# Kernel tuning notes

Measured on AMD Instinct MI355X. Metric: run time of the kernel, lower is better.

Reference implementation:

```python
import jax, jax.numpy as jnp
import numpy as np

TK, HA = 3, 8          # num_blocks, num_heads
AVGF = 32              # num_submatrices
LN_EPS = 1e-5


def _layernorm(x, g, b):
    m = jnp.mean(x, axis=-1, keepdims=True)
    v = jnp.mean((x - m) ** 2, axis=-1, keepdims=True)
    return (x - m) / jnp.sqrt(v + LN_EPS) * g + b


def setup_inputs() -> dict:
    key = jax.random.key(0)
    ks = jax.random.split(key, 12)
    A, B, T = 16, 128, 512
    M = A * B              # 2048
    Dh = M // HA           # 256
    H = 4 * M              # 8192
    s = 0.05               # scale randn params so activations stay finite
    return {
        "x": jax.random.normal(ks[0], (A, B, T), jnp.float32),
        "weight": jax.random.normal(ks[1], (M, M), jnp.float32) * s,
        "Wq": jax.random.normal(ks[2], (TK, HA, Dh, M), jnp.float32) * s,
        "Wk": jax.random.normal(ks[3], (TK, HA, Dh, M), jnp.float32) * s,
        "Wv": jax.random.normal(ks[4], (TK, HA, Dh, M), jnp.float32) * s,
        "Wo": jax.random.normal(ks[5], (TK, M, M), jnp.float32) * s,
        "ln1_g": jnp.ones((M,), jnp.float32),
        "ln1_b": jnp.zeros((M,), jnp.float32),
        "ln2_g": jnp.ones((M,), jnp.float32),
        "ln2_b": jnp.zeros((M,), jnp.float32),
        "fc1_w": jax.random.normal(ks[6], (H, M), jnp.float32) * 0.02,
        "fc1_b": jnp.zeros((H,), jnp.float32),
        "fc2_w": jax.random.normal(ks[7], (M, H), jnp.float32) * 0.02,
        "fc2_b": jnp.zeros((M,), jnp.float32),
    }


def reference(x, weight, Wq, Wk, Wv, Wo, ln1_g, ln1_b, ln2_g, ln2_b,
              fc1_w, fc1_b, fc2_w, fc2_b):
    A, B, T = x.shape
    M = A * B
    Dh = M // HA
    seg = T // AVGF
    # redefine(): transpose(0,2) -> (T,B,A), segment-average along time, flatten
    xt = jnp.transpose(x, (2, 1, 0))                       # (T, B, A)
    xc = xt.reshape(AVGF, seg, B, A).mean(axis=1)          # (AVGF, B, A)
    xcf = xc.reshape(AVGF, M)                              # (AVGF, M)
    # savespace[i] = weight @ x[i]  + sinusoidal positional bias
    pos = jnp.arange(AVGF, dtype=jnp.float32)[:, None]
    je = jnp.arange(0, M, 2, dtype=jnp.float32)
    ang = pos / (10000.0 ** (2.0 * je / M))                # (AVGF, M/2)
    bias = jnp.zeros((AVGF, M), jnp.float32)
    bias = bias.at[:, 0::2].set(jnp.sin(ang)).at[:, 1::2].set(jnp.cos(ang))
    s0 = xcf @ weight.T + bias                             # (AVGF, M)
    scale = 1.0 / jnp.sqrt(jnp.float32(Dh))

    # Sequential recurrence over tokens: vcum[a] carries the cumulative
    # softmax-weighted V sum (softmax over a scalar == 1) per block/head.
    def step(vcum, s):
        for a in range(TK):
            xn = _layernorm(s, ln1_g, ln1_b)
            q = jnp.einsum('hdm,m->hd', Wq[a], xn)         # (HA, Dh)
            k = jnp.einsum('hdm,m->hd', Wk[a], xn)
            v = jnp.einsum('hdm,m->hd', Wv[a], xn)
            scores = jnp.sum(q * k, axis=-1) * scale       # (HA,) scalars
            w = jax.nn.softmax(scores[:, None], axis=-1)[:, 0]  # ones
            vcum = vcum.at[a].add(w[:, None] * v)
            s = Wo[a] @ vcum[a].reshape(-1) + s
            s = _layernorm(s, ln2_g, ln2_b) + s
            h = jax.nn.gelu(fc1_w @ s + fc1_b, approximate=False)
            s = fc2_w @ h + fc2_b
        return vcum, s

    vcum0 = jnp.zeros((TK, HA, Dh), s0.dtype)
    _, out = jax.lax.scan(step, vcum0, s0)                 # (AVGF, M)
    return out.reshape(AVGF, B, A)
```

## Files before the change

kernel.cpp:

```cpp
#include <hip/hip_runtime.h>
#include <math.h>

typedef __attribute__((ext_vector_type(8))) short short8;
typedef __attribute__((ext_vector_type(4))) float floatx4;

__device__ inline unsigned f2bf1(float f) {
    union { float f; unsigned u; } v; v.f = f;
    return (v.u + 0x8000u) >> 16;
}

__device__ inline short8 pack8(float4 a, float4 b) {
    short8 r;
    r[0] = (short)f2bf1(a.x); r[1] = (short)f2bf1(a.y);
    r[2] = (short)f2bf1(a.z); r[3] = (short)f2bf1(a.w);
    r[4] = (short)f2bf1(b.x); r[5] = (short)f2bf1(b.y);
    r[6] = (short)f2bf1(b.z); r[7] = (short)f2bf1(b.w);
    return r;
}

__device__ inline float gelu1(float x) {
    return 0.5f * x * (1.0f + erff(x * 0.70710678118654752f));
}

__global__ __launch_bounds__(128) void avg_k(const float* __restrict__ x,
                                             float* __restrict__ xcf) {
    int blk = blockIdx.x;
    int a = blk >> 7, b = blk & 127;
    int t = threadIdx.x;
    const float4 v = *(const float4*)(x + ((size_t)a * 128 + b) * 512 + t * 4);
    float s = v.x + v.y + v.z + v.w;
    s += __shfl_xor(s, 1);
    s += __shfl_xor(s, 2);
    if ((t & 3) == 0) {
        int seg = t >> 2;
        xcf[seg * 2048 + b * 16 + a] = s * (1.0f / 16.0f);
    }
}

__global__ __launch_bounds__(256) void stats_k(const float* __restrict__ Sin,
                                               float* __restrict__ st) {
    __shared__ float red[8];
    const int row = blockIdx.x, t = threadIdx.x;
    const float* xr = Sin + (size_t)row * 2048;
    float4 v0 = *(const float4*)(xr + t * 4);
    float4 v1 = *(const float4*)(xr + 1024 + t * 4);
    float s = v0.x + v0.y + v0.z + v0.w + v1.x + v1.y + v1.z + v1.w;
    for (int o = 32; o; o >>= 1) s += __shfl_down(s, o);
    if ((t & 63) == 0) red[t >> 6] = s;
    __syncthreads();
    float mean = (red[0] + red[1] + red[2] + red[3]) * (1.0f / 2048.0f);
    float d0 = v0.x - mean, d1 = v0.y - mean, d2 = v0.z - mean, d3 = v0.w - mean;
    float e0 = v1.x - mean, e1 = v1.y - mean, e2 = v1.z - mean, e3 = v1.w - mean;
    float s2 = d0*d0 + d1*d1 + d2*d2 + d3*d3 + e0*e0 + e1*e1 + e2*e2 + e3*e3;
    for (int o = 32; o; o >>= 1) s2 += __shfl_down(s2, o);
    if ((t & 63) == 0) red[4 + (t >> 6)] = s2;
    __syncthreads();
    if (t == 0) {
        float var = (red[4] + red[5] + red[6] + red[7]) * (1.0f / 2048.0f);
        st[row * 2]     = mean;
        st[row * 2 + 1] = 1.0f / sqrtf(var + 1e-5f);
    }
}

template<int KCHUNK, int NT, int STAGE, int EPI>
__global__ __launch_bounds__(256) void gemm_k(const float* __restrict__ X,
                                              const float* __restrict__ W,
                                              float* __restrict__ C,
                                              const float* __restrict__ ebias,
                                              const float* __restrict__ stats,
                                              const float* __restrict__ sg,
                                              const float* __restrict__ sb,
                                              int N, int K) {
    constexpr int PITCH = KCHUNK + 8;
    __shared__ unsigned short Xs[32 * PITCH];
    const int tid = threadIdx.x;
    const int bx = blockIdx.x, by = blockIdx.y;
    const int kb0 = by * KCHUNK;

    if constexpr (STAGE == 2) {
        for (int c = tid; c < KCHUNK; c += 256) {
            const float* vp = X + kb0 + c;
            float run = 0.f;
#pragma unroll
            for (int r = 0; r < 32; r++) {
                run += vp[(size_t)r * K];
                Xs[r * PITCH + c] = (unsigned short)f2bf1(run);
            }
        }
    } else {
        constexpr int NF4 = 32 * (KCHUNK / 4);
        for (int f = tid; f < NF4; f += 256) {
            const int row = f / (KCHUNK / 4), c4 = f % (KCHUNK / 4);
            const int k0 = kb0 + c4 * 4;
            float4 v = *(const float4*)(X + (size_t)row * K + k0);
            if constexpr (STAGE == 1 || STAGE == 11) {
                const float m = stats[row * 2], rs = stats[row * 2 + 1];
                const float4 gg = *(const float4*)(sg + k0);
                const float4 bb = *(const float4*)(sb + k0);
                float4 o;
                o.x = (v.x - m) * rs * gg.x + bb.x;
                o.y = (v.y - m) * rs * gg.y + bb.y;
                o.z = (v.z - m) * rs * gg.z + bb.z;
                o.w = (v.w - m) * rs * gg.w + bb.w;
                if constexpr (STAGE == 11) {
                    o.x += v.x; o.y += v.y; o.z += v.z; o.w += v.w;
                }
                v = o;
            }
            if constexpr (STAGE == 3) {
                const float4 bb = *(const float4*)(sg + k0);
                v.x = gelu1(v.x + bb.x);
                v.y = gelu1(v.y + bb.y);
                v.z = gelu1(v.z + bb.z);
                v.w = gelu1(v.w + bb.w);
            }
            ushort4 p;
            p.x = (unsigned short)f2bf1(v.x);
            p.y = (unsigned short)f2bf1(v.y);
            p.z = (unsigned short)f2bf1(v.z);
            p.w = (unsigned short)f2bf1(v.w);
            *(ushort4*)&Xs[row * PITCH + c4 * 4] = p;
        }
    }
    __syncthreads();

    const int w = tid >> 6, lane = tid & 63;
    const int q = lane >> 4, r16 = lane & 15;
    const int nb = bx * (NT * 64) + w * (NT * 16);
    floatx4 acc[2][NT] = {};
    const float* wp0 = W + (size_t)(nb + r16) * K + kb0 + q * 8;
    const float* wp1 = W + (size_t)(nb + 16 + r16) * K + kb0 + q * 8;

#pragma unroll
    for (int kk = 0; kk < KCHUNK; kk += 32) {
        short8 a0 = *(const short8*)&Xs[r16 * PITCH + kk + q * 8];
        short8 a1 = *(const short8*)&Xs[(16 + r16) * PITCH + kk + q * 8];
        {
            float4 u0 = *(const float4*)(wp0 + kk);
            float4 u1 = *(const float4*)(wp0 + kk + 4);
            short8 bf = pack8(u0, u1);
            acc[0][0] = __builtin_amdgcn_mfma_f32_16x16x32_bf16(a0, bf, acc[0][0], 0, 0, 0);
            acc[1][0] = __builtin_amdgcn_mfma_f32_16x16x32_bf16(a1, bf, acc[1][0], 0, 0, 0);
        }
        if constexpr (NT == 2) {
            float4 u0 = *(const float4*)(wp1 + kk);
            float4 u1 = *(const float4*)(wp1 + kk + 4);
            short8 bf = pack8(u0, u1);
            acc[0][1] = __builtin_amdgcn_mfma_f32_16x16x32_bf16(a0, bf, acc[0][1], 0, 0, 0);
            acc[1][1] = __builtin_amdgcn_mfma_f32_16x16x32_bf16(a1, bf, acc[1][1], 0, 0, 0);
        }
    }

#pragma unroll
    for (int mt = 0; mt < 2; mt++)
#pragma unroll
        for (int nt = 0; nt < NT; nt++)
#pragma unroll
            for (int e = 0; e < 4; e++) {
                int i = mt * 16 + q * 4 + e;
                int n = nb + nt * 16 + r16;
                float v = acc[mt][nt][e];
                if (EPI == 1 && by == 0) v += ebias[n];
                if (EPI == 2 && by == 0) {
                    int ne = n & ~1;
                    float ang = (float)i * __expf(-(float)ne * (9.210340371976184f / 1024.0f));
                    v += (n & 1) ? cosf(ang) : sinf(ang);
                }
                atomicAdd(C + (size_t)i * N + n, v);
            }
}

extern "C" void kernel_launch(void* const* d_in, const int* in_sizes, int n_in,
                              void* d_out, int out_size, void* d_ws, size_t ws_size,
                              hipStream_t stream) {
    const float* x      = (const float*)d_in[0];
    const float* weight = (const float*)d_in[1];
    const float* Wv     = (const float*)d_in[4];
    const float* Wo     = (const float*)d_in[5];
    const float* ln1g   = (const float*)d_in[6];
    const float* ln1b   = (const float*)d_in[7];
    const float* ln2g   = (const float*)d_in[8];
    const float* ln2b   = (const float*)d_in[9];
    const float* fc1w   = (const float*)d_in[10];
    const float* fc1b   = (const float*)d_in[11];
    const float* fc2w   = (const float*)d_in[12];
    const float* fc2b   = (const float*)d_in[13];
    float* ws  = (float*)d_ws;
    float* xcf = ws;
    float* S   = ws + 65536;
    float* V   = ws + 131072;
    float* H   = ws + 196608;
    float* st1 = ws + 458752;
    float* st2 = ws + 458816;
    float* out = (float*)d_out;

    avg_k<<<2048, 128, 0, stream>>>(x, xcf);

    hipMemsetAsync(S, 0, 65536 * 4, stream);
    gemm_k<128, 1, 0, 2><<<dim3(32, 16), 256, 0, stream>>>(
        xcf, weight, S, nullptr, nullptr, nullptr, nullptr, 2048, 2048);

    for (int a = 0; a < 3; a++) {
        stats_k<<<32, 256, 0, stream>>>(S, st1);
        hipMemsetAsync(V, 0, 65536 * 4, stream);
        gemm_k<128, 1, 1, 0><<<dim3(32, 16), 256, 0, stream>>>(
            S, Wv + (size_t)a * 4194304, V, nullptr, st1, ln1g, ln1b, 2048, 2048);
        gemm_k<128, 1, 2, 0><<<dim3(32, 16), 256, 0, stream>>>(
            V, Wo + (size_t)a * 4194304, S, nullptr, nullptr, nullptr, nullptr, 2048, 2048);
        stats_k<<<32, 256, 0, stream>>>(S, st2);
        hipMemsetAsync(H, 0, 262144 * 4, stream);
        gemm_k<256, 1, 11, 0><<<dim3(128, 8), 256, 0, stream>>>(
            S, fc1w, H, nullptr, st2, ln2g, ln2b, 8192, 2048);
        float* Co = (a == 2) ? out : S;
        hipMemsetAsync(Co, 0, 65536 * 4, stream);
        gemm_k<256, 1, 3, 1><<<dim3(32, 32), 256, 0, stream>>>(
            H, fc2w, Co, fc2b, nullptr, fc1b, nullptr, 2048, 8192);
    }
}
```

Measured before the change: 458.6 us.

## Prefetch weight tiles into registers before X staging and halve K chunks

The GEMM kernel now issues all of its weight global loads into registers at kernel start, before the shared-memory staging of the activation rows, so weight streaming overlaps the X conversion and barrier. K chunk sizes are halved and grid split-K doubled, giving more blocks to spread weight bandwidth across CUs. The V and H zeroing memsets are merged into one contiguous memset, and the unused NT template parameter is removed. The cost is more atomicAdd traffic into the outputs from the larger split-K and higher register use for the prefetched weights.

```diff
diff --git a/kernel.cpp b/kernel.cpp
--- a/kernel.cpp
+++ b/kernel.cpp
@@ -62,7 +62,7 @@
     }
 }
 
-template<int KCHUNK, int NT, int STAGE, int EPI>
+template<int KCHUNK, int STAGE, int EPI>
 __global__ __launch_bounds__(256) void gemm_k(const float* __restrict__ X,
                                               const float* __restrict__ W,
                                               float* __restrict__ C,
@@ -76,6 +76,18 @@
     const int tid = threadIdx.x;
     const int bx = blockIdx.x, by = blockIdx.y;
     const int kb0 = by * KCHUNK;
+    const int w = tid >> 6, lane = tid & 63;
+    const int q = lane >> 4, r16 = lane & 15;
+    const int nb = bx * 64 + w * 16;
+
+    constexpr int KI = KCHUNK / 32;
+    const float* wp0 = W + (size_t)(nb + r16) * K + kb0 + q * 8;
+    float4 wr0[KI], wr1[KI];
+#pragma unroll
+    for (int ki = 0; ki < KI; ki++) {
+        wr0[ki] = *(const float4*)(wp0 + ki * 32);
+        wr1[ki] = *(const float4*)(wp0 + ki * 32 + 4);
+    }
 
     if constexpr (STAGE == 2) {
         for (int c = tid; c < KCHUNK; c += 256) {
@@ -124,50 +136,31 @@
     }
     __syncthreads();
 
-    const int w = tid >> 6, lane = tid & 63;
-    const int q = lane >> 4, r16 = lane & 15;
-    const int nb = bx * (NT * 64) + w * (NT * 16);
-    floatx4 acc[2][NT] = {};
-    const float* wp0 = W + (size_t)(nb + r16) * K + kb0 + q * 8;
-    const float* wp1 = W + (size_t)(nb + 16 + r16) * K + kb0 + q * 8;
-
-#pragma unroll
-    for (int kk = 0; kk < KCHUNK; kk += 32) {
-        short8 a0 = *(const short8*)&Xs[r16 * PITCH + kk + q * 8];
-        short8 a1 = *(const short8*)&Xs[(16 + r16) * PITCH + kk + q * 8];
-        {
-            float4 u0 = *(const float4*)(wp0 + kk);
-            float4 u1 = *(const float4*)(wp0 + kk + 4);
-            short8 bf = pack8(u0, u1);
-            acc[0][0] = __builtin_amdgcn_mfma_f32_16x16x32_bf16(a0, bf, acc[0][0], 0, 0, 0);
-            acc[1][0] = __builtin_amdgcn_mfma_f32_16x16x32_bf16(a1, bf, acc[1][0], 0, 0, 0);
+    floatx4 acc0 = {}, acc1 = {};
+#pragma unroll
+    for (int ki = 0; ki < KI; ki++) {
+        short8 a0 = *(const short8*)&Xs[r16 * PITCH + ki * 32 + q * 8];
+        short8 a1 = *(const short8*)&Xs[(16 + r16) * PITCH + ki * 32 + q * 8];
+        short8 bf = pack8(wr0[ki], wr1[ki]);
+        acc0 = __builtin_amdgcn_mfma_f32_16x16x32_bf16(a0, bf, acc0, 0, 0, 0);
+        acc1 = __builtin_amdgcn_mfma_f32_16x16x32_bf16(a1, bf, acc1, 0, 0, 0);
+    }
+
+#pragma unroll
+    for (int mt = 0; mt < 2; mt++)
+#pragma unroll
+        for (int e = 0; e < 4; e++) {
+            int i = mt * 16 + q * 4 + e;
+            int n = nb + r16;
+            float v = (mt == 0) ? acc0[e] : acc1[e];
+            if (EPI == 1 && by == 0) v += ebias[n];
+            if (EPI == 2 && by == 0) {
+                int ne = n & ~1;
+                float ang = (float)i * __expf(-(float)ne * (9.210340371976184f / 1024.0f));
+                v += (n & 1) ? cosf(ang) : sinf(ang);
+            }
+            atomicAdd(C + (size_t)i * N + n, v);
         }
-        if constexpr (NT == 2) {
-            float4 u0 = *(const float4*)(wp1 + kk);
-            float4 u1 = *(const float4*)(wp1 + kk + 4);
-            short8 bf = pack8(u0, u1);
-            acc[0][1] = __builtin_amdgcn_mfma_f32_16x16x32_bf16(a0, bf, acc[0][1], 0, 0, 0);
-            acc[1][1] = __builtin_amdgcn_mfma_f32_16x16x32_bf16(a1, bf, acc[1][1], 0, 0, 0);
-        }
-    }
-
-#pragma unroll
-    for (int mt = 0; mt < 2; mt++)
-#pragma unroll
-        for (int nt = 0; nt < NT; nt++)
-#pragma unroll
-            for (int e = 0; e < 4; e++) {
-                int i = mt * 16 + q * 4 + e;
-                int n = nb + nt * 16 + r16;
-                float v = acc[mt][nt][e];
-                if (EPI == 1 && by == 0) v += ebias[n];
-                if (EPI == 2 && by == 0) {
-                    int ne = n & ~1;
-                    float ang = (float)i * __expf(-(float)ne * (9.210340371976184f / 1024.0f));
-                    v += (n & 1) ? cosf(ang) : sinf(ang);
-                }
-                atomicAdd(C + (size_t)i * N + n, v);
-            }
 }
 
 extern "C" void kernel_launch(void* const* d_in, const int* in_sizes, int n_in,
@@ -197,23 +190,22 @@
     avg_k<<<2048, 128, 0, stream>>>(x, xcf);
 
     hipMemsetAsync(S, 0, 65536 * 4, stream);
-    gemm_k<128, 1, 0, 2><<<dim3(32, 16), 256, 0, stream>>>(
+    gemm_k<64, 0, 2><<<dim3(32, 32), 256, 0, stream>>>(
         xcf, weight, S, nullptr, nullptr, nullptr, nullptr, 2048, 2048);
 
     for (int a = 0; a < 3; a++) {
         stats_k<<<32, 256, 0, stream>>>(S, st1);
-        hipMemsetAsync(V, 0, 65536 * 4, stream);
-        gemm_k<128, 1, 1, 0><<<dim3(32, 16), 256, 0, stream>>>(
+        hipMemsetAsync(V, 0, (65536 + 262144) * 4, stream);
+        gemm_k<64, 1, 0><<<dim3(32, 32), 256, 0, stream>>>(
             S, Wv + (size_t)a * 4194304, V, nullptr, st1, ln1g, ln1b, 2048, 2048);
-        gemm_k<128, 1, 2, 0><<<dim3(32, 16), 256, 0, stream>>>(
+        gemm_k<64, 2, 0><<<dim3(32, 32), 256, 0, stream>>>(
             V, Wo + (size_t)a * 4194304, S, nullptr, nullptr, nullptr, nullptr, 2048, 2048);
         stats_k<<<32, 256, 0, stream>>>(S, st2);
-        hipMemsetAsync(H, 0, 262144 * 4, stream);
-        gemm_k<256, 1, 11, 0><<<dim3(128, 8), 256, 0, stream>>>(
+        gemm_k<128, 11, 0><<<dim3(128, 16), 256, 0, stream>>>(
             S, fc1w, H, nullptr, st2, ln2g, ln2b, 8192, 2048);
         float* Co = (a == 2) ? out : S;
         hipMemsetAsync(Co, 0, 65536 * 4, stream);
-        gemm_k<256, 1, 3, 1><<<dim3(32, 32), 256, 0, stream>>>(
+        gemm_k<128, 3, 1><<<dim3(32, 64), 256, 0, stream>>>(
             H, fc2w, Co, fc2b, nullptr, fc1b, nullptr, 2048, 8192);
     }
 }
```

After: 484.3 us. 5.6% more time.
